# Kernel tuning notes

Measured on AMD Instinct MI355X. Metric: run time of the kernel, lower is better.

## Reference

```python
import jax, jax.numpy as jnp
import numpy as np

B, S, D = 2, 2048, 2048
H, KVH = 32, 8
HD = D // H            # 64
N_REP = H // KVH       # 4
THETA = 10000.0


def _rope_tables(seq_len, half_dim):
    inv = 1.0 / (THETA ** (np.arange(0, half_dim, dtype=np.float32) * 2.0 / (2 * half_dim)))
    t = np.arange(seq_len, dtype=np.float32)
    f = np.outer(t, inv)  # (S, half_dim)
    return jnp.asarray(np.cos(f)), jnp.asarray(np.sin(f))


def setup_inputs() -> dict:
    key = jax.random.key(0)
    ks = jax.random.split(key, 5)
    sc = 0.02
    x = jax.random.normal(ks[0], (B, S, D), dtype=jnp.float32)
    W_q = jax.random.normal(ks[1], (D, H * HD), dtype=jnp.float32) * sc
    W_k = jax.random.normal(ks[2], (D, KVH * HD), dtype=jnp.float32) * sc
    W_v = jax.random.normal(ks[3], (D, KVH * HD), dtype=jnp.float32) * sc
    W_o = jax.random.normal(ks[4], (D, D), dtype=jnp.float32) * sc
    b_o = jnp.zeros((D,), dtype=jnp.float32)
    freqs_cos, freqs_sin = _rope_tables(S, HD // 2)
    return {"x": x, "W_q": W_q, "W_k": W_k, "W_v": W_v, "W_o": W_o,
            "b_o": b_o, "freqs_cos": freqs_cos, "freqs_sin": freqs_sin}


def _apply_rope(t, cos, sin):
    # t: (B, S, h, HD); cos/sin: (S, HD//2), broadcast over batch/heads
    t1, t2 = t[..., 0::2], t[..., 1::2]
    c = cos[None, :, None, :]
    s = sin[None, :, None, :]
    r1 = t1 * c - t2 * s
    r2 = t1 * s + t2 * c
    # interleave back to (..., HD)
    return jnp.stack([r1, r2], axis=-1).reshape(t.shape)


def reference(x, W_q, W_k, W_v, W_o, b_o, freqs_cos, freqs_sin):
    b, s, _ = x.shape
    Q = (x @ W_q).reshape(b, s, H, HD)
    K = (x @ W_k).reshape(b, s, KVH, HD)
    V = (x @ W_v).reshape(b, s, KVH, HD)
    Q = _apply_rope(Q, freqs_cos, freqs_sin)
    K = _apply_rope(K, freqs_cos, freqs_sin)
    # GQA: repeat KV heads (matches torch repeat_interleave along head dim)
    K = jnp.repeat(K, N_REP, axis=2)  # (b, s, H, HD)
    V = jnp.repeat(V, N_REP, axis=2)
    scores = jnp.einsum('bqhd,bkhd->bhqk', Q, K) / jnp.sqrt(jnp.float32(HD))
    causal = jnp.triu(jnp.ones((s, s), dtype=bool), k=1)
    scores = jnp.where(causal[None, None, :, :], -jnp.inf, scores)
    attn = jax.nn.softmax(scores, axis=-1)  # dropout=0 / eval mode -> identity
    ctx = jnp.einsum('bhqk,bkhd->bqhd', attn, V).reshape(b, s, D)
    return ctx @ W_o + b_o
```

## Files before the change

### kernel.cpp

```cpp
#include <hip/hip_runtime.h>
#include <hip/hip_bf16.h>

#define BB 2
#define SS 2048
#define DD 2048
#define HH 32
#define KVH 8
#define HD 64
#define QKV_LD 3072

typedef unsigned short u16;
typedef unsigned int u32;
typedef __attribute__((ext_vector_type(8))) short s16x8;
typedef __attribute__((ext_vector_type(4))) float f32x4;
typedef __attribute__((ext_vector_type(4))) u16 u16x4;
typedef __attribute__((ext_vector_type(2))) u32 u32x2;

#define MFMA(a, b, c) __builtin_amdgcn_mfma_f32_16x16x32_bf16((a), (b), (c), 0, 0, 0)

__device__ __forceinline__ u16 f2bf(float f) {
  union { float f; u32 u; } x; x.f = f;
  u32 r = x.u + 0x7fffu + ((x.u >> 16) & 1u);
  return (u16)(r >> 16);
}
__device__ __forceinline__ float bf2f(u32 u) {
  union { u32 u; float f; } x; x.u = u << 16;
  return x.f;
}
__device__ __forceinline__ u32 cvtpk(float a, float b) {
  u32 r;
  asm("v_cvt_pk_bf16_f32 %0, %1, %2" : "=v"(r) : "v"(a), "v"(b));
  return r;
}

__device__ __forceinline__ void gload16(const void* g, void* l) {
  __builtin_amdgcn_global_load_lds((const __attribute__((address_space(1))) unsigned int*)g,
                                   (__attribute__((address_space(3))) unsigned int*)l, 16, 0, 0);
}

__device__ __forceinline__ s16x8 lds_frag(const u16* base, int row, int c) {
  return *(const s16x8*)(base + (row << 6) + (((c ^ (row & 7)) << 3)));
}

__global__ void cast_bf(const float* __restrict__ s, u16* __restrict__ d) {
  int i = blockIdx.x * 256 + threadIdx.x;
  float4 v = ((const float4*)s)[i];
  u16x4 o;
  o[0] = f2bf(v.x); o[1] = f2bf(v.y); o[2] = f2bf(v.z); o[3] = f2bf(v.w);
  ((u16x4*)d)[i] = o;
}

__global__ void tcast(const float* __restrict__ src, int scols, u16* __restrict__ dst, int dld) {
  __shared__ float tt[32][33];
  int c0 = blockIdx.x << 5, r0 = blockIdx.y << 5;
  int tx = threadIdx.x, ty = threadIdx.y;
#pragma unroll
  for (int j = 0; j < 4; ++j)
    tt[ty + j * 8][tx] = src[(size_t)(r0 + ty + j * 8) * scols + c0 + tx];
  __syncthreads();
#pragma unroll
  for (int j = 0; j < 4; ++j)
    dst[(size_t)(c0 + ty + j * 8) * dld + r0 + tx] = f2bf(tt[tx][ty + j * 8]);
}

__global__ void rope_k(u16* __restrict__ qkv, const float* __restrict__ fc, const float* __restrict__ fs) {
  const float SCLQ = 0.125f * 1.44269504f;
  int idx = blockIdx.x * 256 + threadIdx.x;
  int row = idx / 1280;
  int p = idx - row * 1280;
  int s = row & (SS - 1);
  int col, i;
  float sc;
  if (p < 1024) { col = p << 1; i = p & 31; sc = SCLQ; }
  else { int pk = p - 1024; col = 2048 + (pk << 1); i = pk & 31; sc = 1.0f; }
  size_t base = (size_t)row * QKV_LD + col;
  u32 v = *(const u32*)(qkv + base);
  float t1 = bf2f(v & 0xffffu), t2 = bf2f(v >> 16);
  float c = fc[s * 32 + i], sn = fs[s * 32 + i];
  float r1 = (t1 * c - t2 * sn) * sc;
  float r2 = (t1 * sn + t2 * c) * sc;
  *(u32*)(qkv + base) = (u32)f2bf(r1) | ((u32)f2bf(r2) << 16);
}

__global__ void transpose_v(const u16* __restrict__ qkv, u16* __restrict__ vt) {
  __shared__ u16 tt[32][33];
  int c0 = blockIdx.x << 5, r0 = blockIdx.y << 5;
  int tx = threadIdx.x, ty = threadIdx.y;
#pragma unroll
  for (int j = 0; j < 4; ++j)
    tt[ty + j * 8][tx] = qkv[(size_t)(r0 + ty + j * 8) * QKV_LD + 2560 + c0 + tx];
  __syncthreads();
#pragma unroll
  for (int j = 0; j < 4; ++j) {
    int c = c0 + ty + j * 8;
    int rr = r0 + tx;
    int b = rr >> 11, s = rr & (SS - 1), g = c >> 6, d = c & 63;
    vt[(size_t)((((b << 3) + g) << 6) + d) * SS + s] = tt[tx][ty + j * 8];
  }
}

__global__ __launch_bounds__(512) void gemm_bt(const u16* __restrict__ A, const u16* __restrict__ BT,
                                               int K, u16* __restrict__ Cb, float* __restrict__ Cf,
                                               const float* __restrict__ bias, int ldc) {
  __shared__ alignas(16) u16 lds[2 * 128 * 64];
  u16* Al = lds;
  u16* Bl = lds + 128 * 64;
  const int t = threadIdx.x, w = t >> 6, lane = t & 63;
  const int q_l = lane & 15, gh = lane >> 4;
  const int m0 = blockIdx.y << 7, n0 = blockIdx.x << 7;
  const int wm = (w >> 2) << 6;
  const int wn = (w & 3) << 5;
  f32x4 acc[4][2] = {};

  for (int k0 = 0; k0 < K; k0 += 64) {
#pragma unroll
    for (int i = 0; i < 2; ++i) {
      int o = (i << 13) + (t << 4);
      int row = o >> 7;
      int cs = ((((o >> 4) & 7) ^ (row & 7)) << 4);
      gload16((const char*)A + (((size_t)(m0 + row) * K + k0) << 1) + cs, (char*)Al + o);
      gload16((const char*)BT + (((size_t)(n0 + row) * K + k0) << 1) + cs, (char*)Bl + o);
    }
    __syncthreads();
#pragma unroll
    for (int kk = 0; kk < 64; kk += 32) {
      const int c = (kk >> 3) + gh;
      s16x8 af[4], bfr[2];
#pragma unroll
      for (int mi = 0; mi < 4; ++mi) af[mi] = lds_frag(Al, wm + (mi << 4) + q_l, c);
#pragma unroll
      for (int ni = 0; ni < 2; ++ni) bfr[ni] = lds_frag(Bl, wn + (ni << 4) + q_l, c);
#pragma unroll
      for (int mi = 0; mi < 4; ++mi)
#pragma unroll
        for (int ni = 0; ni < 2; ++ni)
          acc[mi][ni] = MFMA(af[mi], bfr[ni], acc[mi][ni]);
    }
    __syncthreads();
  }

  const int rbase = m0 + wm + (gh << 2);
  const int cbase = n0 + wn + q_l;
  if (Cf != nullptr) {
#pragma unroll
    for (int mi = 0; mi < 4; ++mi)
#pragma unroll
      for (int ni = 0; ni < 2; ++ni) {
        int col = cbase + (ni << 4);
        float bv = bias[col];
#pragma unroll
        for (int r = 0; r < 4; ++r)
          Cf[(size_t)(rbase + (mi << 4) + r) * ldc + col] = acc[mi][ni][r] + bv;
      }
  } else {
#pragma unroll
    for (int mi = 0; mi < 4; ++mi)
#pragma unroll
      for (int ni = 0; ni < 2; ++ni) {
        int col = cbase + (ni << 4);
#pragma unroll
        for (int r = 0; r < 4; ++r)
          Cb[(size_t)(rbase + (mi << 4) + r) * ldc + col] = f2bf(acc[mi][ni][r]);
      }
  }
}

__global__ __launch_bounds__(256) void attn_k(const u16* __restrict__ qkv, const u16* __restrict__ vt,
                                              u16* __restrict__ ctx) {
  __shared__ alignas(16) u16 sK[64 * 64];
  __shared__ alignas(16) u16 sV[64 * 64];
  __shared__ alignas(16) u16 sP[4][16 * 64];
  const int bid = blockIdx.x;
  const int qt = 31 - (bid >> 6);
  const int h = bid & 31, b = (bid >> 5) & 1;
  const int q0 = qt << 6, g = h >> 2;
  const int t = threadIdx.x, w = t >> 6, lane = t & 63;
  const int q_l = lane & 15, gh = lane >> 4;

  const s16x8 ones = { (short)0x3F80, (short)0x3F80, (short)0x3F80, (short)0x3F80,
                       (short)0x3F80, (short)0x3F80, (short)0x3F80, (short)0x3F80 };

  const int srow = (w << 3) + (lane >> 3);
  const int blk = lane & 7;
  const int lw0 = (srow << 6) + ((blk ^ (lane >> 3)) << 3);
  const u16* kg = qkv + (size_t)((b << 11) + srow) * QKV_LD + 2048 + (g << 6) + (blk << 3);
  const u16* vg = vt + (size_t)((((b << 3) + g) << 6) + srow) * SS + (blk << 3);

  const int qrow = (b << 11) + q0 + (w << 4) + q_l;
  const u16* qptr = qkv + (size_t)qrow * QKV_LD + (h << 6) + (gh << 3);
  s16x8 qa0 = *(const s16x8*)qptr;
  s16x8 qa1 = *(const s16x8*)(qptr + 32);

  f32x4 o[4] = {};
  f32x4 lacc = {};
  float m1 = -INFINITY;
  const int myq = q0 + (w << 4) + q_l;

  s16x8 kr[2], vr[2];
#pragma unroll
  for (int i = 0; i < 2; ++i) {
    kr[i] = *(const s16x8*)(kg + (size_t)(i << 5) * QKV_LD);
    vr[i] = *(const s16x8*)(vg + (size_t)(i << 5) * SS);
  }
#pragma unroll
  for (int i = 0; i < 2; ++i) {
    *(s16x8*)(sK + lw0 + (i << 11)) = kr[i];
    *(s16x8*)(sV + lw0 + (i << 11)) = vr[i];
  }
  __syncthreads();

  for (int kt_i = 0; kt_i <= qt; ++kt_i) {
    const int k0 = kt_i << 6;
    if (kt_i < qt) {
      const int kn = k0 + 64;
#pragma unroll
      for (int i = 0; i < 2; ++i) {
        kr[i] = *(const s16x8*)(kg + (size_t)(kn + (i << 5)) * QKV_LD);
        vr[i] = *(const s16x8*)(vg + (size_t)(i << 5) * SS + kn);
      }
    }

    f32x4 sacc[4];
    __builtin_amdgcn_s_setprio(1);
#pragma unroll
    for (int nc = 0; nc < 4; ++nc) {
      f32x4 a = {};
      a = MFMA(lds_frag(sK, (nc << 4) + q_l, gh), qa0, a);
      a = MFMA(lds_frag(sK, (nc << 4) + q_l, 4 + gh), qa1, a);
      sacc[nc] = a;
    }
    __builtin_amdgcn_s_setprio(0);

    float pv[4][4];
    if (kt_i == qt) {
#pragma unroll
      for (int nc = 0; nc < 4; ++nc) {
        int kb = k0 + (nc << 4) + (gh << 2);
#pragma unroll
        for (int r = 0; r < 4; ++r) {
          float v = sacc[nc][r];
          if (kb + r > myq) v = -INFINITY;
          pv[nc][r] = v;
        }
      }
    } else {
#pragma unroll
      for (int nc = 0; nc < 4; ++nc)
#pragma unroll
        for (int r = 0; r < 4; ++r)
          pv[nc][r] = sacc[nc][r];
    }

    float ta = fmaxf(fmaxf(pv[0][0], pv[0][1]), pv[0][2]);
    float tb = fmaxf(fmaxf(pv[0][3], pv[1][0]), pv[1][1]);
    float tc = fmaxf(fmaxf(pv[1][2], pv[1][3]), pv[2][0]);
    float td = fmaxf(fmaxf(pv[2][1], pv[2][2]), pv[2][3]);
    float te = fmaxf(fmaxf(pv[3][0], pv[3][1]), pv[3][2]);
    float tmax = fmaxf(fmaxf(fmaxf(ta, tb), fmaxf(tc, td)), fmaxf(te, pv[3][3]));
    if (__any(tmax > m1 + 8.f)) {
      float rmax = tmax;
      rmax = fmaxf(rmax, __shfl_xor(rmax, 16));
      rmax = fmaxf(rmax, __shfl_xor(rmax, 32));
      float mn = fmaxf(m1, rmax);
      float alpha = exp2f(m1 - mn);
      m1 = mn;
#pragma unroll
      for (int r = 0; r < 4; ++r) lacc[r] *= alpha;
#pragma unroll
      for (int dc = 0; dc < 4; ++dc)
#pragma unroll
        for (int r = 0; r < 4; ++r) o[dc][r] *= alpha;
    }

#pragma unroll
    for (int nc = 0; nc < 4; ++nc)
#pragma unroll
      for (int r = 0; r < 4; ++r)
        pv[nc][r] = exp2f(pv[nc][r] - m1);

    u16* pb = sP[w];
#pragma unroll
    for (int nc = 0; nc < 4; ++nc) {
      u32x2 pw;
      pw[0] = cvtpk(pv[nc][0], pv[nc][1]);
      pw[1] = cvtpk(pv[nc][2], pv[nc][3]);
      int byte = (q_l << 7) + (((((nc << 1) + (gh >> 1)) ^ (q_l & 7)) << 4)) + ((gh & 1) << 3);
      *(u32x2*)((char*)pb + byte) = pw;
    }
    asm volatile("s_waitcnt lgkmcnt(0)" ::: "memory");
    __builtin_amdgcn_sched_barrier(0);

    s16x8 pa0 = lds_frag(pb, q_l, gh);
    s16x8 pa1 = lds_frag(pb, q_l, 4 + gh);
    __builtin_amdgcn_s_setprio(1);
#pragma unroll
    for (int dc = 0; dc < 4; ++dc) {
      o[dc] = MFMA(lds_frag(sV, (dc << 4) + q_l, gh), pa0, o[dc]);
      o[dc] = MFMA(lds_frag(sV, (dc << 4) + q_l, 4 + gh), pa1, o[dc]);
    }
    lacc = MFMA(ones, pa0, lacc);
    lacc = MFMA(ones, pa1, lacc);
    __builtin_amdgcn_s_setprio(0);

    __syncthreads();
    if (kt_i < qt) {
#pragma unroll
      for (int i = 0; i < 2; ++i) {
        *(s16x8*)(sK + lw0 + (i << 11)) = kr[i];
        *(s16x8*)(sV + lw0 + (i << 11)) = vr[i];
      }
      __syncthreads();
    }
  }

  float inv = 1.0f / lacc[0];
  u16* crow = ctx + (size_t)((b << 11) + myq) * DD + (h << 6) + (gh << 2);
#pragma unroll
  for (int dc = 0; dc < 4; ++dc) {
    u32x2 ov;
    ov[0] = cvtpk(o[dc][0] * inv, o[dc][1] * inv);
    ov[1] = cvtpk(o[dc][2] * inv, o[dc][3] * inv);
    *(u32x2*)(crow + (dc << 4)) = ov;
  }
}

extern "C" void kernel_launch(void* const* d_in, const int* in_sizes, int n_in,
                              void* d_out, int out_size, void* d_ws, size_t ws_size,
                              hipStream_t stream) {
  const float* x  = (const float*)d_in[0];
  const float* Wq = (const float*)d_in[1];
  const float* Wk = (const float*)d_in[2];
  const float* Wv = (const float*)d_in[3];
  const float* Wo = (const float*)d_in[4];
  const float* bo = (const float*)d_in[5];
  const float* fc = (const float*)d_in[6];
  const float* fs = (const float*)d_in[7];
  float* out = (float*)d_out;

  u16* ws   = (u16*)d_ws;
  u16* xb   = ws;
  u16* wT   = xb + 8388608;
  u16* qkv  = wT + 6291456;
  u16* vt   = qkv + 12582912;
  u16* ctx  = xb;
  u16* woT  = wT;

  dim3 b32(32, 8, 1);

  cast_bf<<<8192, 256, 0, stream>>>(x, xb);
  tcast<<<dim3(64, 64), b32, 0, stream>>>(Wq, 2048, wT, 2048);
  tcast<<<dim3(16, 64), b32, 0, stream>>>(Wk, 512, wT + (size_t)2048 * 2048, 2048);
  tcast<<<dim3(16, 64), b32, 0, stream>>>(Wv, 512, wT + (size_t)2560 * 2048, 2048);

  gemm_bt<<<dim3(24, 32), 512, 0, stream>>>(xb, wT, 2048, qkv, nullptr, nullptr, QKV_LD);

  tcast<<<dim3(64, 64), b32, 0, stream>>>(Wo, 2048, woT, 2048);

  rope_k<<<20480, 256, 0, stream>>>(qkv, fc, fs);
  transpose_v<<<dim3(16, 128), b32, 0, stream>>>(qkv, vt);

  attn_k<<<2048, 256, 0, stream>>>(qkv, vt, ctx);

  gemm_bt<<<dim3(16, 32), 512, 0, stream>>>(ctx, woT, 2048, nullptr, out, bo, 2048);
}
```

Before: 218.4 us.

## Process two query tiles per attention block and vectorize RoPE kernel

The attention kernel now handles 128 query rows per block as two 64-row sets, A and B. Each K/V tile loaded into LDS is reused by both sets, which halves K/V global traffic and the number of blocks, at the cost of more registers and fewer blocks to spread across CUs. The RoPE kernel now has each thread process four rotary pairs using 16-byte loads and stores, with the conversion done by the packed bf16 instruction.

```diff
diff --git a/kernel.cpp b/kernel.cpp
--- a/kernel.cpp
+++ b/kernel.cpp
@@ -15,6 +15,7 @@
 typedef __attribute__((ext_vector_type(4))) float f32x4;
 typedef __attribute__((ext_vector_type(4))) u16 u16x4;
 typedef __attribute__((ext_vector_type(2))) u32 u32x2;
+typedef __attribute__((ext_vector_type(4))) u32 u32x4;
 
 #define MFMA(a, b, c) __builtin_amdgcn_mfma_f32_16x16x32_bf16((a), (b), (c), 0, 0, 0)
 
@@ -66,20 +67,28 @@
 __global__ void rope_k(u16* __restrict__ qkv, const float* __restrict__ fc, const float* __restrict__ fs) {
   const float SCLQ = 0.125f * 1.44269504f;
   int idx = blockIdx.x * 256 + threadIdx.x;
-  int row = idx / 1280;
-  int p = idx - row * 1280;
+  int row = idx / 320;
+  int p4 = (idx - row * 320) << 2;
   int s = row & (SS - 1);
   int col, i;
   float sc;
-  if (p < 1024) { col = p << 1; i = p & 31; sc = SCLQ; }
-  else { int pk = p - 1024; col = 2048 + (pk << 1); i = pk & 31; sc = 1.0f; }
+  if (p4 < 1024) { col = p4 << 1; i = p4 & 31; sc = SCLQ; }
+  else { int pk = p4 - 1024; col = 2048 + (pk << 1); i = pk & 31; sc = 1.0f; }
   size_t base = (size_t)row * QKV_LD + col;
-  u32 v = *(const u32*)(qkv + base);
-  float t1 = bf2f(v & 0xffffu), t2 = bf2f(v >> 16);
-  float c = fc[s * 32 + i], sn = fs[s * 32 + i];
-  float r1 = (t1 * c - t2 * sn) * sc;
-  float r2 = (t1 * sn + t2 * c) * sc;
-  *(u32*)(qkv + base) = (u32)f2bf(r1) | ((u32)f2bf(r2) << 16);
+  u32x4 v = *(const u32x4*)(qkv + base);
+  const float4 c4 = *(const float4*)(fc + s * 32 + i);
+  const float4 s4 = *(const float4*)(fs + s * 32 + i);
+  float cc[4] = {c4.x, c4.y, c4.z, c4.w};
+  float ss[4] = {s4.x, s4.y, s4.z, s4.w};
+  u32x4 o;
+#pragma unroll
+  for (int j = 0; j < 4; ++j) {
+    float t1 = bf2f(v[j] & 0xffffu), t2 = bf2f(v[j] >> 16);
+    float r1 = (t1 * cc[j] - t2 * ss[j]) * sc;
+    float r2 = (t1 * ss[j] + t2 * cc[j]) * sc;
+    o[j] = cvtpk(r1, r2);
+  }
+  *(u32x4*)(qkv + base) = o;
 }
 
 __global__ void transpose_v(const u16* __restrict__ qkv, u16* __restrict__ vt) {
@@ -169,13 +178,15 @@
                                               u16* __restrict__ ctx) {
   __shared__ alignas(16) u16 sK[64 * 64];
   __shared__ alignas(16) u16 sV[64 * 64];
-  __shared__ alignas(16) u16 sP[4][16 * 64];
+  __shared__ alignas(16) u16 sPa[4][16 * 64];
+  __shared__ alignas(16) u16 sPb[4][16 * 64];
   const int bid = blockIdx.x;
-  const int qt = 31 - (bid >> 6);
+  const int qt2 = 15 - (bid >> 6);
   const int h = bid & 31, b = (bid >> 5) & 1;
-  const int q0 = qt << 6, g = h >> 2;
+  const int q0 = qt2 << 7, g = h >> 2;
   const int t = threadIdx.x, w = t >> 6, lane = t & 63;
   const int q_l = lane & 15, gh = lane >> 4;
+  const int diagA = qt2 << 1, ktmax = (qt2 << 1) + 1;
 
   const s16x8 ones = { (short)0x3F80, (short)0x3F80, (short)0x3F80, (short)0x3F80,
                        (short)0x3F80, (short)0x3F80, (short)0x3F80, (short)0x3F80 };
@@ -186,53 +197,35 @@
   const u16* kg = qkv + (size_t)((b << 11) + srow) * QKV_LD + 2048 + (g << 6) + (blk << 3);
   const u16* vg = vt + (size_t)((((b << 3) + g) << 6) + srow) * SS + (blk << 3);
 
-  const int qrow = (b << 11) + q0 + (w << 4) + q_l;
-  const u16* qptr = qkv + (size_t)qrow * QKV_LD + (h << 6) + (gh << 3);
-  s16x8 qa0 = *(const s16x8*)qptr;
-  s16x8 qa1 = *(const s16x8*)(qptr + 32);
-
-  f32x4 o[4] = {};
-  f32x4 lacc = {};
-  float m1 = -INFINITY;
-  const int myq = q0 + (w << 4) + q_l;
-
-  s16x8 kr[2], vr[2];
-#pragma unroll
-  for (int i = 0; i < 2; ++i) {
-    kr[i] = *(const s16x8*)(kg + (size_t)(i << 5) * QKV_LD);
-    vr[i] = *(const s16x8*)(vg + (size_t)(i << 5) * SS);
-  }
-#pragma unroll
-  for (int i = 0; i < 2; ++i) {
-    *(s16x8*)(sK + lw0 + (i << 11)) = kr[i];
-    *(s16x8*)(sV + lw0 + (i << 11)) = vr[i];
-  }
-  __syncthreads();
-
-  for (int kt_i = 0; kt_i <= qt; ++kt_i) {
-    const int k0 = kt_i << 6;
-    if (kt_i < qt) {
-      const int kn = k0 + 64;
-#pragma unroll
-      for (int i = 0; i < 2; ++i) {
-        kr[i] = *(const s16x8*)(kg + (size_t)(kn + (i << 5)) * QKV_LD);
-        vr[i] = *(const s16x8*)(vg + (size_t)(i << 5) * SS + kn);
-      }
-    }
-
+  const int qrowA = (b << 11) + q0 + (w << 4) + q_l;
+  const u16* qptrA = qkv + (size_t)qrowA * QKV_LD + (h << 6) + (gh << 3);
+  s16x8 qa0 = *(const s16x8*)qptrA;
+  s16x8 qa1 = *(const s16x8*)(qptrA + 32);
+  const u16* qptrB = qptrA + (size_t)64 * QKV_LD;
+  s16x8 qb0 = *(const s16x8*)qptrB;
+  s16x8 qb1 = *(const s16x8*)(qptrB + 32);
+
+  f32x4 oA[4] = {}, oB[4] = {};
+  f32x4 lA = {}, lB = {};
+  float mA = -INFINITY, mB = -INFINITY;
+  const int myqA = q0 + (w << 4) + q_l;
+  const int myqB = myqA + 64;
+
+  auto doset = [&](const s16x8& qf0, const s16x8& qf1, f32x4 (&o)[4], f32x4& lac,
+                   float& m1, int myq, bool diag, u16* pb, int k0) {
     f32x4 sacc[4];
     __builtin_amdgcn_s_setprio(1);
 #pragma unroll
     for (int nc = 0; nc < 4; ++nc) {
       f32x4 a = {};
-      a = MFMA(lds_frag(sK, (nc << 4) + q_l, gh), qa0, a);
-      a = MFMA(lds_frag(sK, (nc << 4) + q_l, 4 + gh), qa1, a);
+      a = MFMA(lds_frag(sK, (nc << 4) + q_l, gh), qf0, a);
+      a = MFMA(lds_frag(sK, (nc << 4) + q_l, 4 + gh), qf1, a);
       sacc[nc] = a;
     }
     __builtin_amdgcn_s_setprio(0);
 
     float pv[4][4];
-    if (kt_i == qt) {
+    if (diag) {
 #pragma unroll
       for (int nc = 0; nc < 4; ++nc) {
         int kb = k0 + (nc << 4) + (gh << 2);
@@ -265,7 +258,7 @@
       float alpha = exp2f(m1 - mn);
       m1 = mn;
 #pragma unroll
-      for (int r = 0; r < 4; ++r) lacc[r] *= alpha;
+      for (int r = 0; r < 4; ++r) lac[r] *= alpha;
 #pragma unroll
       for (int dc = 0; dc < 4; ++dc)
 #pragma unroll
@@ -278,7 +271,6 @@
       for (int r = 0; r < 4; ++r)
         pv[nc][r] = exp2f(pv[nc][r] - m1);
 
-    u16* pb = sP[w];
 #pragma unroll
     for (int nc = 0; nc < 4; ++nc) {
       u32x2 pw;
@@ -298,12 +290,41 @@
       o[dc] = MFMA(lds_frag(sV, (dc << 4) + q_l, gh), pa0, o[dc]);
       o[dc] = MFMA(lds_frag(sV, (dc << 4) + q_l, 4 + gh), pa1, o[dc]);
     }
-    lacc = MFMA(ones, pa0, lacc);
-    lacc = MFMA(ones, pa1, lacc);
+    lac = MFMA(ones, pa0, lac);
+    lac = MFMA(ones, pa1, lac);
     __builtin_amdgcn_s_setprio(0);
+  };
+
+  s16x8 kr[2], vr[2];
+#pragma unroll
+  for (int i = 0; i < 2; ++i) {
+    kr[i] = *(const s16x8*)(kg + (size_t)(i << 5) * QKV_LD);
+    vr[i] = *(const s16x8*)(vg + (size_t)(i << 5) * SS);
+  }
+#pragma unroll
+  for (int i = 0; i < 2; ++i) {
+    *(s16x8*)(sK + lw0 + (i << 11)) = kr[i];
+    *(s16x8*)(sV + lw0 + (i << 11)) = vr[i];
+  }
+  __syncthreads();
+
+  for (int kt_i = 0; kt_i <= ktmax; ++kt_i) {
+    const int k0 = kt_i << 6;
+    if (kt_i < ktmax) {
+      const int kn = k0 + 64;
+#pragma unroll
+      for (int i = 0; i < 2; ++i) {
+        kr[i] = *(const s16x8*)(kg + (size_t)(kn + (i << 5)) * QKV_LD);
+        vr[i] = *(const s16x8*)(vg + (size_t)(i << 5) * SS + kn);
+      }
+    }
+
+    if (kt_i <= diagA)
+      doset(qa0, qa1, oA, lA, mA, myqA, kt_i == diagA, sPa[w], k0);
+    doset(qb0, qb1, oB, lB, mB, myqB, kt_i == ktmax, sPb[w], k0);
 
     __syncthreads();
-    if (kt_i < qt) {
+    if (kt_i < ktmax) {
 #pragma unroll
       for (int i = 0; i < 2; ++i) {
         *(s16x8*)(sK + lw0 + (i << 11)) = kr[i];
@@ -313,14 +334,20 @@
     }
   }
 
-  float inv = 1.0f / lacc[0];
-  u16* crow = ctx + (size_t)((b << 11) + myq) * DD + (h << 6) + (gh << 2);
+  float invA = 1.0f / lA[0];
+  float invB = 1.0f / lB[0];
+  u16* crowA = ctx + (size_t)((b << 11) + myqA) * DD + (h << 6) + (gh << 2);
+  u16* crowB = ctx + (size_t)((b << 11) + myqB) * DD + (h << 6) + (gh << 2);
 #pragma unroll
   for (int dc = 0; dc < 4; ++dc) {
     u32x2 ov;
-    ov[0] = cvtpk(o[dc][0] * inv, o[dc][1] * inv);
-    ov[1] = cvtpk(o[dc][2] * inv, o[dc][3] * inv);
-    *(u32x2*)(crow + (dc << 4)) = ov;
+    ov[0] = cvtpk(oA[dc][0] * invA, oA[dc][1] * invA);
+    ov[1] = cvtpk(oA[dc][2] * invA, oA[dc][3] * invA);
+    *(u32x2*)(crowA + (dc << 4)) = ov;
+    u32x2 ow;
+    ow[0] = cvtpk(oB[dc][0] * invB, oB[dc][1] * invB);
+    ow[1] = cvtpk(oB[dc][2] * invB, oB[dc][3] * invB);
+    *(u32x2*)(crowB + (dc << 4)) = ow;
   }
 }
 
@@ -356,10 +383,10 @@
 
   tcast<<<dim3(64, 64), b32, 0, stream>>>(Wo, 2048, woT, 2048);
 
-  rope_k<<<20480, 256, 0, stream>>>(qkv, fc, fs);
+  rope_k<<<5120, 256, 0, stream>>>(qkv, fc, fs);
   transpose_v<<<dim3(16, 128), b32, 0, stream>>>(qkv, vt);
 
-  attn_k<<<2048, 256, 0, stream>>>(qkv, vt, ctx);
+  attn_k<<<1024, 256, 0, stream>>>(qkv, vt, ctx);
 
   gemm_bt<<<dim3(16, 32), 512, 0, stream>>>(ctx, woT, 2048, nullptr, out, bo, 2048);
 }
```

After: 229.0 us. 4.9% more time.
